# Kernel tuning notes

Hardware: AMD Instinct MI355X
Metric: run time of the kernel (lower is better)

## Reference

```python
import jax, jax.numpy as jnp
import numpy as np

K = 4  # correlation radius -> (2K+1)**2 = 81 displacement channels


def setup_inputs() -> dict:
    key = jax.random.key(0)
    kx, ky = jax.random.split(key)
    x = jax.random.normal(kx, (4, 64, 256, 256), dtype=jnp.float32)
    y = jax.random.normal(ky, (4, 64, 256, 256), dtype=jnp.float32)
    return {"x": x, "y": y}


def reference(x, y):
    b, c, ph, pw = x.shape
    k = K
    # reflect-pad y by k on both spatial dims (matches F.pad(..., 'reflect'))
    yp = jnp.pad(y, ((0, 0), (0, 0), (k, k), (k, k)), mode="reflect")
    # fixed 81-offset loop (trace-time); each term: channel-sum correlation
    outs = [
        jnp.sum(x * jax.lax.dynamic_slice(yp, (0, 0, k + i, k + j), (b, c, ph, pw)), axis=1)
        for i in range(-k, k + 1)
        for j in range(-k, k + 1)
    ]
    return jnp.stack(outs, axis=1)  # [b, (2k+1)^2, ph, pw]
```

## Files before the change

kernel.cpp:

```cpp
#include <hip/hip_runtime.h>


#define HH   256
#define WW   256
#define CCH  64
#define KRAD 4
#define ND   81

#define WT   16
#define HT   16
#define WY   24
#define RSTRIDE 128
#define YRING 10
#define YSLOT (WY * RSTRIDE)
#define PSTRIDE 72

typedef __attribute__((ext_vector_type(8))) short bf16x8;
typedef __attribute__((ext_vector_type(4))) float f32x4;

__device__ __forceinline__ int reflect(int v, int n) {
    v = v < 0 ? -v : v;
    return v >= n ? 2 * n - 2 - v : v;
}
__device__ __forceinline__ unsigned f2bf_pk(float a, float b) {
    union { float f; unsigned u; } xa, xb;
    xa.f = a; xb.f = b;
    unsigned ra = (xa.u + 0x7fffu + ((xa.u >> 16) & 1u)) >> 16;
    unsigned rb = (xb.u + 0x7fffu + ((xb.u >> 16) & 1u)) >> 16;
    return ra | (rb << 16);
}
__device__ __forceinline__ int mod10(int s) {
    if (s >= 20) s -= 20; else if (s >= 10) s -= 10;
    return s;
}

__global__ __launch_bounds__(256, 4) void corr_mfma_kernel(
    const float* __restrict__ x, const float* __restrict__ y,
    float* __restrict__ out)
{
    __shared__ char lds[YRING * YSLOT + ND * PSTRIDE + 12];
    char* ylds   = lds;
    char* pstage = lds + YRING * YSLOT;

    const int d  = blockIdx.x;
    const int v  = (d & 7) * 128 + (d >> 3);
    const int b  = v >> 8;
    const int by = (v >> 4) & 15;
    const int bx = v & 15;
    const int w0 = bx * WT;
    const int h0 = by * HT;

    const int t    = threadIdx.x;
    const int wid  = t >> 6;
    const int lane = t & 63;
    const int lq   = lane >> 4;
    const int ln   = lane & 15;

    const size_t plane = (size_t)HH * WW;
    const float* yb = y + (size_t)b * CCH * plane;
    const float* xb = x + (size_t)b * CCH * plane;

    const int yp  = t & 31;
    const int ycg = t >> 5;

    auto loadY = [&](int hrow, float* v8) {
        int gh = reflect(hrow, HH);
        int pc = yp < WY ? yp : WY - 1;
        int gw = reflect(w0 - KRAD + pc, WW);
        const float* src = yb + (size_t)(ycg * 8) * plane + (size_t)gh * WW + gw;
#pragma unroll
        for (int j = 0; j < 8; ++j) v8[j] = src[(size_t)j * plane];
    };
    auto writeY = [&](int slot, const float* v8) {
        if (yp < WY) {
            char* dst = ylds + slot * YSLOT + yp * RSTRIDE
                      + (((unsigned)(ycg * 16)) ^ ((unsigned)(yp & 7) << 4));
            union { unsigned u[4]; uint4 q; } pk;
#pragma unroll
            for (int m = 0; m < 4; ++m)
                pk.u[m] = f2bf_pk(v8[2 * m], v8[2 * m + 1]);
            *(uint4*)dst = pk.q;
        }
    };
    auto loadX = [&](int hrow, float* v16) {
        int gh = reflect(hrow, HH);
        const float* src = xb + (size_t)(lq * 8) * plane + (size_t)gh * WW + (w0 + ln);
#pragma unroll
        for (int j = 0; j < 8; ++j) v16[j] = src[(size_t)j * plane];
        const float* src2 = src + (size_t)32 * plane;
#pragma unroll
        for (int j = 0; j < 8; ++j) v16[8 + j] = src2[(size_t)j * plane];
    };
    auto xconv = [&](const float* v16, bf16x8& f0, bf16x8& f1) {
        union { unsigned u[4]; bf16x8 v; } c0, c1;
#pragma unroll
        for (int m = 0; m < 4; ++m) {
            c0.u[m] = f2bf_pk(v16[2 * m], v16[2 * m + 1]);
            c1.u[m] = f2bf_pk(v16[8 + 2 * m], v16[9 + 2 * m]);
        }
        f0 = c0.v; f1 = c1.v;
    };

    float yv[8], yv2[8], xv[16];
    bf16x8 bf0, bf1;

    loadY(h0 - KRAD, yv);
    loadX(h0, xv);
#pragma unroll 1
    for (int j = 0; j < 9; ++j) {
        if (j < 8) loadY(h0 - KRAD + j + 1, yv2);
        writeY(j, yv);
#pragma unroll
        for (int m = 0; m < 8; ++m) yv[m] = yv2[m];
    }
    xconv(xv, bf0, bf1);
    __syncthreads();

    const int mbase = lq * 4;
    const int prow  = t >> 4;
    const int pcol  = t & 15;

#pragma unroll 1
    for (int hh = 0; hh < HT; ++hh) {
        const int h = h0 + hh;

        loadY(h + KRAD + 1, yv);
        loadX(h + 1, xv);

        for (int u = wid; u < 18; u += 4) {
            const int di = u >> 1;
            const int wt = u & 1;
            const int slot = mod10(hh + di);
            const char* abase = ylds + slot * YSLOT + (wt * 16 + ln) * RSTRIDE;
            const unsigned sw = (unsigned)(ln & 7) << 4;
            bf16x8 af0 = *(const bf16x8*)(abase + (((unsigned)(lq * 16)) ^ sw));
            bf16x8 af1 = *(const bf16x8*)(abase + (((unsigned)(64 + lq * 16)) ^ sw));
            f32x4 dacc = {0.f, 0.f, 0.f, 0.f};
            dacc = __builtin_amdgcn_mfma_f32_16x16x32_bf16(af0, bf0, dacc, 0, 0, 0);
            dacc = __builtin_amdgcn_mfma_f32_16x16x32_bf16(af1, bf1, dacc, 0, 0, 0);
            char* psu = pstage + di * (9 * PSTRIDE) + ln * 4;
#pragma unroll
            for (int r = 0; r < 4; ++r) {
                const int vr = mbase + r - ln + (wt ? 16 : 0);
                if ((unsigned)vr <= 8u)
                    *(float*)(psu + vr * PSTRIDE) = dacc[r];
            }
        }

        writeY(mod10(hh + 9), yv);
        xconv(xv, bf0, bf1);

        __builtin_amdgcn_sched_barrier(0);
        asm volatile("s_waitcnt lgkmcnt(0)" ::: "memory");
        __builtin_amdgcn_s_barrier();
        __builtin_amdgcn_sched_barrier(0);

        {
            float* og = out + (size_t)b * ND * plane + (size_t)h * WW + (w0 + pcol);
#pragma unroll
            for (int p = 0; p < 6; ++p) {
                const int didx = p * 16 + prow;
                if (p < 5 || prow == 0) {
                    float vv = *(const float*)(pstage + didx * PSTRIDE + pcol * 4);
                    og[(size_t)didx * plane] = vv;
                }
            }
        }

        __builtin_amdgcn_sched_barrier(0);
        __builtin_amdgcn_s_barrier();
        __builtin_amdgcn_sched_barrier(0);
    }
}

extern "C" void kernel_launch(void* const* d_in, const int* in_sizes, int n_in,
                              void* d_out, int out_size, void* d_ws, size_t ws_size,
                              hipStream_t stream) {
    const float* x = (const float*)d_in[0];
    const float* y = (const float*)d_in[1];
    float* out = (float*)d_out;

    dim3 grid(1024);
    dim3 block(256);
    corr_mfma_kernel<<<grid, block, 0, stream>>>(x, y, out);
}
```

Before: 57.70 us.

## Process two output rows per iteration with vectorized epilogue and deeper prefetch

Restructures the main loop so each iteration computes two output rows, which halves the number of barrier pairs and doubles the MFMA work between syncs. The x/y prefetch now covers two rows ahead. Displacement 80 is written straight to global memory so the staging buffer fits exactly 80 rows per output row. The epilogue uses 8-byte vector stores. This adds register pressure from the doubled prefetch buffers, which may hurt occupancy at launch_bounds 4, and the direct store of the 81st channel is scattered.

```diff
diff --git a/kernel.cpp b/kernel.cpp
--- a/kernel.cpp
+++ b/kernel.cpp
@@ -9,14 +9,18 @@
 
 #define WT   16
 #define HT   16
+#define NEP  8
 #define WY   24
 #define RSTRIDE 128
 #define YRING 10
 #define YSLOT (WY * RSTRIDE)
-#define PSTRIDE 72
+#define PRS   64
+#define PROWS 80
+#define PSLOT (PROWS * PRS)
 
 typedef __attribute__((ext_vector_type(8))) short bf16x8;
 typedef __attribute__((ext_vector_type(4))) float f32x4;
+typedef __attribute__((ext_vector_type(2))) float f32x2;
 
 __device__ __forceinline__ int reflect(int v, int n) {
     v = v < 0 ? -v : v;
@@ -38,7 +42,7 @@
     const float* __restrict__ x, const float* __restrict__ y,
     float* __restrict__ out)
 {
-    __shared__ char lds[YRING * YSLOT + ND * PSTRIDE + 12];
+    __shared__ char lds[YRING * YSLOT + 2 * PSLOT];
     char* ylds   = lds;
     char* pstage = lds + YRING * YSLOT;
 
@@ -59,21 +63,22 @@
     const size_t plane = (size_t)HH * WW;
     const float* yb = y + (size_t)b * CCH * plane;
     const float* xb = x + (size_t)b * CCH * plane;
+    float* outb = out + (size_t)b * ND * plane;
 
     const int yp  = t & 31;
     const int ycg = t >> 5;
 
-    auto loadY = [&](int hrow, float* v8) {
-        int gh = reflect(hrow, HH);
+    auto loadY = [&](int L, float* v8) {
+        int gh = reflect(h0 - KRAD + L, HH);
         int pc = yp < WY ? yp : WY - 1;
         int gw = reflect(w0 - KRAD + pc, WW);
         const float* src = yb + (size_t)(ycg * 8) * plane + (size_t)gh * WW + gw;
 #pragma unroll
         for (int j = 0; j < 8; ++j) v8[j] = src[(size_t)j * plane];
     };
-    auto writeY = [&](int slot, const float* v8) {
+    auto writeY = [&](int L, const float* v8) {
         if (yp < WY) {
-            char* dst = ylds + slot * YSLOT + yp * RSTRIDE
+            char* dst = ylds + mod10(L) * YSLOT + yp * RSTRIDE
                       + (((unsigned)(ycg * 16)) ^ ((unsigned)(yp & 7) << 4));
             union { unsigned u[4]; uint4 q; } pk;
 #pragma unroll
@@ -101,73 +106,90 @@
         f0 = c0.v; f1 = c1.v;
     };
 
-    float yv[8], yv2[8], xv[16];
-    bf16x8 bf0, bf1;
-
-    loadY(h0 - KRAD, yv);
-    loadX(h0, xv);
+    float yv[8], yv2[8], yva[8], yvb[8], xva[16], xvb[16];
+    bf16x8 bfA0, bfA1, bfB0, bfB1;
+
+    const int mbase = lq * 4;
+    const unsigned sw = ((unsigned)(ln & 7)) << 4;
+
+    loadY(0, yv);
 #pragma unroll 1
-    for (int j = 0; j < 9; ++j) {
-        if (j < 8) loadY(h0 - KRAD + j + 1, yv2);
+    for (int j = 0; j < 10; ++j) {
+        if (j < 9) loadY(j + 1, yv2);
         writeY(j, yv);
 #pragma unroll
         for (int m = 0; m < 8; ++m) yv[m] = yv2[m];
     }
-    xconv(xv, bf0, bf1);
+    loadX(h0, xva);
+    loadX(h0 + 1, xvb);
     __syncthreads();
 
-    const int mbase = lq * 4;
-    const int prow  = t >> 4;
-    const int pcol  = t & 15;
-
 #pragma unroll 1
-    for (int hh = 0; hh < HT; ++hh) {
-        const int h = h0 + hh;
-
-        loadY(h + KRAD + 1, yv);
-        loadX(h + 1, xv);
+    for (int ep = 0; ep < NEP; ++ep) {
+        const int h = h0 + 2 * ep;
+        const bool pf = (ep < NEP - 1);
+
+        if (pf) { loadY(2 * ep + 10, yva); loadY(2 * ep + 11, yvb); }
+        xconv(xva, bfA0, bfA1);
+        xconv(xvb, bfB0, bfB1);
+        if (pf) { loadX(h + 2, xva); loadX(h + 3, xvb); }
 
         for (int u = wid; u < 18; u += 4) {
             const int di = u >> 1;
             const int wt = u & 1;
-            const int slot = mod10(hh + di);
-            const char* abase = ylds + slot * YSLOT + (wt * 16 + ln) * RSTRIDE;
-            const unsigned sw = (unsigned)(ln & 7) << 4;
-            bf16x8 af0 = *(const bf16x8*)(abase + (((unsigned)(lq * 16)) ^ sw));
-            bf16x8 af1 = *(const bf16x8*)(abase + (((unsigned)(64 + lq * 16)) ^ sw));
-            f32x4 dacc = {0.f, 0.f, 0.f, 0.f};
-            dacc = __builtin_amdgcn_mfma_f32_16x16x32_bf16(af0, bf0, dacc, 0, 0, 0);
-            dacc = __builtin_amdgcn_mfma_f32_16x16x32_bf16(af1, bf1, dacc, 0, 0, 0);
-            char* psu = pstage + di * (9 * PSTRIDE) + ln * 4;
+            const int s0 = mod10(2 * ep + di);
+            const int s1 = mod10(2 * ep + 1 + di);
+            const char* a0 = ylds + s0 * YSLOT + (wt * 16 + ln) * RSTRIDE;
+            const char* a1 = ylds + s1 * YSLOT + (wt * 16 + ln) * RSTRIDE;
+            bf16x8 af00 = *(const bf16x8*)(a0 + (((unsigned)(lq * 16)) ^ sw));
+            bf16x8 af01 = *(const bf16x8*)(a0 + (((unsigned)(64 + lq * 16)) ^ sw));
+            bf16x8 af10 = *(const bf16x8*)(a1 + (((unsigned)(lq * 16)) ^ sw));
+            bf16x8 af11 = *(const bf16x8*)(a1 + (((unsigned)(64 + lq * 16)) ^ sw));
+            f32x4 d0 = {0.f, 0.f, 0.f, 0.f};
+            f32x4 d1 = {0.f, 0.f, 0.f, 0.f};
+            d0 = __builtin_amdgcn_mfma_f32_16x16x32_bf16(af00, bfA0, d0, 0, 0, 0);
+            d0 = __builtin_amdgcn_mfma_f32_16x16x32_bf16(af01, bfA1, d0, 0, 0, 0);
+            d1 = __builtin_amdgcn_mfma_f32_16x16x32_bf16(af10, bfB0, d1, 0, 0, 0);
+            d1 = __builtin_amdgcn_mfma_f32_16x16x32_bf16(af11, bfB1, d1, 0, 0, 0);
 #pragma unroll
             for (int r = 0; r < 4; ++r) {
-                const int vr = mbase + r - ln + (wt ? 16 : 0);
-                if ((unsigned)vr <= 8u)
-                    *(float*)(psu + vr * PSTRIDE) = dacc[r];
+                const int vrr = mbase + r - ln + (wt ? 16 : 0);
+                if ((unsigned)vrr <= 8u) {
+                    const int didx = di * 9 + vrr;
+                    if (didx < PROWS) {
+                        *(float*)(pstage + didx * PRS + ln * 4) = d0[r];
+                        *(float*)(pstage + PSLOT + didx * PRS + ln * 4) = d1[r];
+                    } else {
+                        outb[(size_t)80 * plane + (size_t)h * WW + (w0 + ln)] = d0[r];
+                        outb[(size_t)80 * plane + (size_t)(h + 1) * WW + (w0 + ln)] = d1[r];
+                    }
+                }
             }
         }
-
-        writeY(mod10(hh + 9), yv);
-        xconv(xv, bf0, bf1);
 
         __builtin_amdgcn_sched_barrier(0);
         asm volatile("s_waitcnt lgkmcnt(0)" ::: "memory");
         __builtin_amdgcn_s_barrier();
         __builtin_amdgcn_sched_barrier(0);
 
+        if (pf) { writeY(2 * ep + 10, yva); writeY(2 * ep + 11, yvb); }
+
         {
-            float* og = out + (size_t)b * ND * plane + (size_t)h * WW + (w0 + pcol);
-#pragma unroll
-            for (int p = 0; p < 6; ++p) {
-                const int didx = p * 16 + prow;
-                if (p < 5 || prow == 0) {
-                    float vv = *(const float*)(pstage + didx * PSTRIDE + pcol * 4);
-                    og[(size_t)didx * plane] = vv;
-                }
+#pragma unroll
+            for (int p = 0; p < 5; ++p) {
+                const int idx = t + 256 * p;
+                const int row = idx >> 3;
+                const int c2  = idx & 7;
+                f32x2 vv = *(const f32x2*)(pstage + row * PRS + c2 * 8);
+                const int didx = (row < PROWS) ? row : row - PROWS;
+                const int hr   = (row < PROWS) ? h : h + 1;
+                *(f32x2*)(outb + (size_t)didx * plane + (size_t)hr * WW
+                          + (w0 + c2 * 2)) = vv;
             }
         }
 
         __builtin_amdgcn_sched_barrier(0);
+        asm volatile("s_waitcnt lgkmcnt(0)" ::: "memory");
         __builtin_amdgcn_s_barrier();
         __builtin_amdgcn_sched_barrier(0);
     }
```

Result: no change. 58.55 us (+1.5%).

## Vectorize global loads of x and y, staging x through double-buffered LDS

Applied to the files above, without the earlier changes.

Replaces the per-thread scalar strided channel loads with 16-byte vector loads along the width dimension for both x and y, plus scalar loads only for the y halo columns. Because each thread now holds one channel rather than eight, data is transposed into the channel-contiguous bf16 layout through scattered 2-byte LDS writes. x now also goes through a double-buffered LDS tile instead of living in registers, and the LDS writes are moved after the first barrier. The intent is to cut global load instruction count and improve coalescing. In exchange it adds many small LDS stores, possible bank conflicts and an extra lgkmcnt wait before the second barrier.

```diff
diff --git a/kernel.cpp b/kernel.cpp
--- a/kernel.cpp
+++ b/kernel.cpp
@@ -13,6 +13,7 @@
 #define RSTRIDE 128
 #define YRING 10
 #define YSLOT (WY * RSTRIDE)
+#define XSLOT (WT * RSTRIDE)
 #define PSTRIDE 72
 
 typedef __attribute__((ext_vector_type(8))) short bf16x8;
@@ -22,12 +23,9 @@
     v = v < 0 ? -v : v;
     return v >= n ? 2 * n - 2 - v : v;
 }
-__device__ __forceinline__ unsigned f2bf_pk(float a, float b) {
-    union { float f; unsigned u; } xa, xb;
-    xa.f = a; xb.f = b;
-    unsigned ra = (xa.u + 0x7fffu + ((xa.u >> 16) & 1u)) >> 16;
-    unsigned rb = (xb.u + 0x7fffu + ((xb.u >> 16) & 1u)) >> 16;
-    return ra | (rb << 16);
+__device__ __forceinline__ unsigned short f2bf(float f) {
+    union { float f; unsigned u; } v; v.f = f;
+    return (unsigned short)((v.u + 0x7fffu + ((v.u >> 16) & 1u)) >> 16);
 }
 __device__ __forceinline__ int mod10(int s) {
     if (s >= 20) s -= 20; else if (s >= 10) s -= 10;
@@ -38,9 +36,10 @@
     const float* __restrict__ x, const float* __restrict__ y,
     float* __restrict__ out)
 {
-    __shared__ char lds[YRING * YSLOT + ND * PSTRIDE + 12];
+    __shared__ char lds[YRING * YSLOT + 2 * XSLOT + ND * PSTRIDE + 12];
     char* ylds   = lds;
-    char* pstage = lds + YRING * YSLOT;
+    char* xlds   = lds + YRING * YSLOT;
+    char* pstage = xlds + 2 * XSLOT;
 
     const int d  = blockIdx.x;
     const int v  = (d & 7) * 128 + (d >> 3);
@@ -60,81 +59,98 @@
     const float* yb = y + (size_t)b * CCH * plane;
     const float* xb = x + (size_t)b * CCH * plane;
 
-    const int yp  = t & 31;
-    const int ycg = t >> 5;
-
-    auto loadY = [&](int hrow, float* v8) {
+    const int yc  = t >> 2, ywc = t & 3;
+    const int yhc = t >> 3, yhk = t & 7;
+    const int yph = (yhk < 4) ? yhk : yhk + 16;
+    const int xc  = t >> 2, xwc = t & 3;
+
+    auto loadYi = [&](int L, f32x4& f4) {
+        int gh = reflect(h0 - KRAD + L, HH);
+        f4 = *(const f32x4*)(yb + (size_t)yc * plane + (size_t)gh * WW + (w0 + ywc * 4));
+    };
+    auto loadYh = [&](int L, float& a, float& bb) {
+        int gh = reflect(h0 - KRAD + L, HH);
+        int gw = reflect(w0 - KRAD + yph, WW);
+        const float* p = yb + (size_t)yhc * plane + (size_t)gh * WW + gw;
+        a  = *p;
+        bb = *(p + (size_t)32 * plane);
+    };
+    auto writeY = [&](int L, const f32x4& f4, float ha, float hb) {
+        char* base = ylds + mod10(L) * YSLOT;
+#pragma unroll
+        for (int e = 0; e < 4; ++e) {
+            int yp = 4 + ywc * 4 + e;
+            char* p = base + yp * RSTRIDE
+                    + ((((unsigned)(yc >> 3)) * 16) ^ (((unsigned)(yp & 7)) << 4))
+                    + (yc & 7) * 2;
+            *(unsigned short*)p = f2bf(f4[e]);
+        }
+        {
+            char* p = base + yph * RSTRIDE
+                    + ((((unsigned)(yhc >> 3)) * 16) ^ (((unsigned)(yph & 7)) << 4))
+                    + (yhc & 7) * 2;
+            *(unsigned short*)p = f2bf(ha);
+            int c2 = yhc + 32;
+            char* p2 = base + yph * RSTRIDE
+                     + ((((unsigned)(c2 >> 3)) * 16) ^ (((unsigned)(yph & 7)) << 4))
+                     + (c2 & 7) * 2;
+            *(unsigned short*)p2 = f2bf(hb);
+        }
+    };
+    auto loadX4 = [&](int hrow, f32x4& f4) {
         int gh = reflect(hrow, HH);
-        int pc = yp < WY ? yp : WY - 1;
-        int gw = reflect(w0 - KRAD + pc, WW);
-        const float* src = yb + (size_t)(ycg * 8) * plane + (size_t)gh * WW + gw;
-#pragma unroll
-        for (int j = 0; j < 8; ++j) v8[j] = src[(size_t)j * plane];
-    };
-    auto writeY = [&](int slot, const float* v8) {
-        if (yp < WY) {
-            char* dst = ylds + slot * YSLOT + yp * RSTRIDE
-                      + (((unsigned)(ycg * 16)) ^ ((unsigned)(yp & 7) << 4));
-            union { unsigned u[4]; uint4 q; } pk;
-#pragma unroll
-            for (int m = 0; m < 4; ++m)
-                pk.u[m] = f2bf_pk(v8[2 * m], v8[2 * m + 1]);
-            *(uint4*)dst = pk.q;
-        }
-    };
-    auto loadX = [&](int hrow, float* v16) {
-        int gh = reflect(hrow, HH);
-        const float* src = xb + (size_t)(lq * 8) * plane + (size_t)gh * WW + (w0 + ln);
-#pragma unroll
-        for (int j = 0; j < 8; ++j) v16[j] = src[(size_t)j * plane];
-        const float* src2 = src + (size_t)32 * plane;
-#pragma unroll
-        for (int j = 0; j < 8; ++j) v16[8 + j] = src2[(size_t)j * plane];
-    };
-    auto xconv = [&](const float* v16, bf16x8& f0, bf16x8& f1) {
-        union { unsigned u[4]; bf16x8 v; } c0, c1;
-#pragma unroll
-        for (int m = 0; m < 4; ++m) {
-            c0.u[m] = f2bf_pk(v16[2 * m], v16[2 * m + 1]);
-            c1.u[m] = f2bf_pk(v16[8 + 2 * m], v16[9 + 2 * m]);
-        }
-        f0 = c0.v; f1 = c1.v;
-    };
-
-    float yv[8], yv2[8], xv[16];
-    bf16x8 bf0, bf1;
-
-    loadY(h0 - KRAD, yv);
-    loadX(h0, xv);
+        f4 = *(const f32x4*)(xb + (size_t)xc * plane + (size_t)gh * WW + (w0 + xwc * 4));
+    };
+    auto writeX4 = [&](int buf, const f32x4& f4) {
+        char* base = xlds + buf * XSLOT;
+#pragma unroll
+        for (int e = 0; e < 4; ++e) {
+            int xp = xwc * 4 + e;
+            char* p = base + xp * RSTRIDE
+                    + ((((unsigned)(xc >> 3)) * 16) ^ (((unsigned)(xp & 7)) << 4))
+                    + (xc & 7) * 2;
+            *(unsigned short*)p = f2bf(f4[e]);
+        }
+    };
+
+    f32x4 yi, yi2, xv4;
+    float ha, hb, ha2, hb2;
+
+    loadYi(0, yi); loadYh(0, ha, hb);
 #pragma unroll 1
     for (int j = 0; j < 9; ++j) {
-        if (j < 8) loadY(h0 - KRAD + j + 1, yv2);
-        writeY(j, yv);
-#pragma unroll
-        for (int m = 0; m < 8; ++m) yv[m] = yv2[m];
+        if (j < 8) { loadYi(j + 1, yi2); loadYh(j + 1, ha2, hb2); }
+        writeY(j, yi, ha, hb);
+        yi = yi2; ha = ha2; hb = hb2;
     }
-    xconv(xv, bf0, bf1);
+    loadX4(h0, xv4);
+    writeX4(0, xv4);
     __syncthreads();
 
     const int mbase = lq * 4;
     const int prow  = t >> 4;
     const int pcol  = t & 15;
+    const unsigned swl = ((unsigned)(ln & 7)) << 4;
 
 #pragma unroll 1
     for (int hh = 0; hh < HT; ++hh) {
-        const int h = h0 + hh;
-
-        loadY(h + KRAD + 1, yv);
-        loadX(h + 1, xv);
+        const int h   = h0 + hh;
+        const int cur = hh & 1;
+
+        loadYi(hh + 9, yi); loadYh(hh + 9, ha, hb);
+        loadX4(h + 1, xv4);
+
+        const char* xrow = xlds + cur * XSLOT + ln * RSTRIDE;
+        bf16x8 bf0 = *(const bf16x8*)(xrow + (((unsigned)(lq * 16)) ^ swl));
+        bf16x8 bf1 = *(const bf16x8*)(xrow + (((unsigned)(64 + lq * 16)) ^ swl));
 
         for (int u = wid; u < 18; u += 4) {
             const int di = u >> 1;
             const int wt = u & 1;
             const int slot = mod10(hh + di);
             const char* abase = ylds + slot * YSLOT + (wt * 16 + ln) * RSTRIDE;
-            const unsigned sw = (unsigned)(ln & 7) << 4;
-            bf16x8 af0 = *(const bf16x8*)(abase + (((unsigned)(lq * 16)) ^ sw));
-            bf16x8 af1 = *(const bf16x8*)(abase + (((unsigned)(64 + lq * 16)) ^ sw));
+            bf16x8 af0 = *(const bf16x8*)(abase + (((unsigned)(lq * 16)) ^ swl));
+            bf16x8 af1 = *(const bf16x8*)(abase + (((unsigned)(64 + lq * 16)) ^ swl));
             f32x4 dacc = {0.f, 0.f, 0.f, 0.f};
             dacc = __builtin_amdgcn_mfma_f32_16x16x32_bf16(af0, bf0, dacc, 0, 0, 0);
             dacc = __builtin_amdgcn_mfma_f32_16x16x32_bf16(af1, bf1, dacc, 0, 0, 0);
@@ -147,13 +163,13 @@
             }
         }
 
-        writeY(mod10(hh + 9), yv);
-        xconv(xv, bf0, bf1);
-
         __builtin_amdgcn_sched_barrier(0);
         asm volatile("s_waitcnt lgkmcnt(0)" ::: "memory");
         __builtin_amdgcn_s_barrier();
         __builtin_amdgcn_sched_barrier(0);
+
+        writeY(hh + 9, yi, ha, hb);
+        writeX4(cur ^ 1, xv4);
 
         {
             float* og = out + (size_t)b * ND * plane + (size_t)h * WW + (w0 + pcol);
@@ -168,6 +184,7 @@
         }
 
         __builtin_amdgcn_sched_barrier(0);
+        asm volatile("s_waitcnt lgkmcnt(0)" ::: "memory");
         __builtin_amdgcn_s_barrier();
         __builtin_amdgcn_sched_barrier(0);
     }
```

Result: slower. 59.68 us (+3.4%).

## Halve row tile, double-buffer X/Y prefetch, shrink LDS for higher occupancy

Applied to the files above, without the earlier changes.

Cuts the rows per block from 16 to 8, which doubles the grid, and drops the Y ring to 9 slots. The main loop is unrolled by two with separate X and Y register buffers, so the loads for later rows are issued before the current row's MFMA work. The partial-result staging buffer is compacted to 80 rows, with displacement 80 written straight to global memory, so LDS use falls and the launch bound can rise to 5 blocks per CU. The trade-off is more redundant halo loads of Y from the smaller tiles, plus extra registers for the doubled buffers.

```diff
diff --git a/kernel.cpp b/kernel.cpp
--- a/kernel.cpp
+++ b/kernel.cpp
@@ -8,12 +8,14 @@
 #define ND   81
 
 #define WT   16
-#define HT   16
+#define HT   8
 #define WY   24
 #define RSTRIDE 128
-#define YRING 10
+#define YRING 9
 #define YSLOT (WY * RSTRIDE)
-#define PSTRIDE 72
+#define PRS   64
+#define PROWS 80
+#define PSLOT (PROWS * PRS)
 
 typedef __attribute__((ext_vector_type(8))) short bf16x8;
 typedef __attribute__((ext_vector_type(4))) float f32x4;
@@ -29,24 +31,23 @@
     unsigned rb = (xb.u + 0x7fffu + ((xb.u >> 16) & 1u)) >> 16;
     return ra | (rb << 16);
 }
-__device__ __forceinline__ int mod10(int s) {
-    if (s >= 20) s -= 20; else if (s >= 10) s -= 10;
-    return s;
-}
-
-__global__ __launch_bounds__(256, 4) void corr_mfma_kernel(
+__device__ __forceinline__ int mod9(int s) {
+    return s >= 9 ? s - 9 : s;
+}
+
+__global__ __launch_bounds__(256, 5) void corr_mfma_kernel(
     const float* __restrict__ x, const float* __restrict__ y,
     float* __restrict__ out)
 {
-    __shared__ char lds[YRING * YSLOT + ND * PSTRIDE + 12];
+    __shared__ char lds[YRING * YSLOT + PSLOT];
     char* ylds   = lds;
     char* pstage = lds + YRING * YSLOT;
 
     const int d  = blockIdx.x;
-    const int v  = (d & 7) * 128 + (d >> 3);
-    const int b  = v >> 8;
-    const int by = (v >> 4) & 15;
+    const int v  = (d & 7) * 256 + (d >> 3);
     const int bx = v & 15;
+    const int by = (v >> 4) & 31;
+    const int b  = v >> 9;
     const int w0 = bx * WT;
     const int h0 = by * HT;
 
@@ -59,21 +60,22 @@
     const size_t plane = (size_t)HH * WW;
     const float* yb = y + (size_t)b * CCH * plane;
     const float* xb = x + (size_t)b * CCH * plane;
+    float* outb = out + (size_t)b * ND * plane;
 
     const int yp  = t & 31;
     const int ycg = t >> 5;
 
-    auto loadY = [&](int hrow, float* v8) {
-        int gh = reflect(hrow, HH);
+    auto loadY = [&](int L, float* v8) {
+        int gh = reflect(h0 - KRAD + L, HH);
         int pc = yp < WY ? yp : WY - 1;
         int gw = reflect(w0 - KRAD + pc, WW);
         const float* src = yb + (size_t)(ycg * 8) * plane + (size_t)gh * WW + gw;
 #pragma unroll
         for (int j = 0; j < 8; ++j) v8[j] = src[(size_t)j * plane];
     };
-    auto writeY = [&](int slot, const float* v8) {
+    auto writeY = [&](int L, const float* v8) {
         if (yp < WY) {
-            char* dst = ylds + slot * YSLOT + yp * RSTRIDE
+            char* dst = ylds + mod9(L) * YSLOT + yp * RSTRIDE
                       + (((unsigned)(ycg * 16)) ^ ((unsigned)(yp & 7) << 4));
             union { unsigned u[4]; uint4 q; } pk;
 #pragma unroll
@@ -101,75 +103,93 @@
         f0 = c0.v; f1 = c1.v;
     };
 
-    float yv[8], yv2[8], xv[16];
-    bf16x8 bf0, bf1;
-
-    loadY(h0 - KRAD, yv);
-    loadX(h0, xv);
-#pragma unroll 1
-    for (int j = 0; j < 9; ++j) {
-        if (j < 8) loadY(h0 - KRAD + j + 1, yv2);
-        writeY(j, yv);
-#pragma unroll
-        for (int m = 0; m < 8; ++m) yv[m] = yv2[m];
-    }
-    xconv(xv, bf0, bf1);
-    __syncthreads();
-
     const int mbase = lq * 4;
     const int prow  = t >> 4;
     const int pcol  = t & 15;
-
-#pragma unroll 1
-    for (int hh = 0; hh < HT; ++hh) {
+    const unsigned swl = ((unsigned)(ln & 7)) << 4;
+
+    auto body = [&](int hh, const bf16x8& bf0, const bf16x8& bf1, const float* yW) {
         const int h = h0 + hh;
-
-        loadY(h + KRAD + 1, yv);
-        loadX(h + 1, xv);
 
         for (int u = wid; u < 18; u += 4) {
             const int di = u >> 1;
             const int wt = u & 1;
-            const int slot = mod10(hh + di);
+            const int slot = mod9(hh + di);
             const char* abase = ylds + slot * YSLOT + (wt * 16 + ln) * RSTRIDE;
-            const unsigned sw = (unsigned)(ln & 7) << 4;
-            bf16x8 af0 = *(const bf16x8*)(abase + (((unsigned)(lq * 16)) ^ sw));
-            bf16x8 af1 = *(const bf16x8*)(abase + (((unsigned)(64 + lq * 16)) ^ sw));
+            bf16x8 af0 = *(const bf16x8*)(abase + (((unsigned)(lq * 16)) ^ swl));
+            bf16x8 af1 = *(const bf16x8*)(abase + (((unsigned)(64 + lq * 16)) ^ swl));
             f32x4 dacc = {0.f, 0.f, 0.f, 0.f};
             dacc = __builtin_amdgcn_mfma_f32_16x16x32_bf16(af0, bf0, dacc, 0, 0, 0);
             dacc = __builtin_amdgcn_mfma_f32_16x16x32_bf16(af1, bf1, dacc, 0, 0, 0);
-            char* psu = pstage + di * (9 * PSTRIDE) + ln * 4;
 #pragma unroll
             for (int r = 0; r < 4; ++r) {
                 const int vr = mbase + r - ln + (wt ? 16 : 0);
-                if ((unsigned)vr <= 8u)
-                    *(float*)(psu + vr * PSTRIDE) = dacc[r];
+                if ((unsigned)vr <= 8u) {
+                    const int didx = di * 9 + vr;
+                    if (didx < PROWS)
+                        *(float*)(pstage + didx * PRS + ln * 4) = dacc[r];
+                    else
+                        outb[(size_t)80 * plane + (size_t)h * WW + (w0 + ln)] = dacc[r];
+                }
             }
         }
-
-        writeY(mod10(hh + 9), yv);
-        xconv(xv, bf0, bf1);
 
         __builtin_amdgcn_sched_barrier(0);
         asm volatile("s_waitcnt lgkmcnt(0)" ::: "memory");
         __builtin_amdgcn_s_barrier();
         __builtin_amdgcn_sched_barrier(0);
 
+        if (hh < HT - 1) writeY(hh + 9, yW);
+
         {
-            float* og = out + (size_t)b * ND * plane + (size_t)h * WW + (w0 + pcol);
-#pragma unroll
-            for (int p = 0; p < 6; ++p) {
+            float* og = outb + (size_t)h * WW + (w0 + pcol);
+#pragma unroll
+            for (int p = 0; p < 5; ++p) {
                 const int didx = p * 16 + prow;
-                if (p < 5 || prow == 0) {
-                    float vv = *(const float*)(pstage + didx * PSTRIDE + pcol * 4);
-                    og[(size_t)didx * plane] = vv;
-                }
+                float vv = *(const float*)(pstage + didx * PRS + pcol * 4);
+                og[(size_t)didx * plane] = vv;
             }
         }
 
         __builtin_amdgcn_sched_barrier(0);
+        asm volatile("s_waitcnt lgkmcnt(0)" ::: "memory");
         __builtin_amdgcn_s_barrier();
         __builtin_amdgcn_sched_barrier(0);
+    };
+
+    float yA[8], yB[8], xvE[16], xvO[16];
+    bf16x8 bf0, bf1;
+
+    loadY(0, yA);
+#pragma unroll 1
+    for (int j = 0; j < 9; ++j) {
+        if (j < 8) loadY(j + 1, yB);
+        writeY(j, yA);
+#pragma unroll
+        for (int m = 0; m < 8; ++m) yA[m] = yB[m];
+    }
+    loadY(9, yA);
+    loadX(h0, xvE);
+    loadX(h0 + 1, xvO);
+    __syncthreads();
+
+#pragma unroll 1
+    for (int e = 0; e < HT / 2; ++e) {
+        const int hh0 = 2 * e;
+
+        xconv(xvE, bf0, bf1);
+        if (hh0 < HT - 2) {
+            loadY(hh0 + 10, yB);
+            loadX(h0 + hh0 + 2, xvE);
+        }
+        body(hh0, bf0, bf1, yA);
+
+        xconv(xvO, bf0, bf1);
+        if (hh0 + 1 < HT - 2) {
+            loadY(hh0 + 11, yA);
+            loadX(h0 + hh0 + 3, xvO);
+        }
+        body(hh0 + 1, bf0, bf1, yB);
     }
 }
 
@@ -180,7 +200,7 @@
     const float* y = (const float*)d_in[1];
     float* out = (float*)d_out;
 
-    dim3 grid(1024);
+    dim3 grid(2048);
     dim3 block(256);
     corr_mfma_kernel<<<grid, block, 0, stream>>>(x, y, out);
 }
```

New measurement: 104.4 us. +81.0%, slower.
